# Optimization experiments

Measured on AMD Instinct MI355X. Metric: run time of the kernel, lower is better.

## Reference

```python
import jax, jax.numpy as jnp
import numpy as np
import math

HIDDEN = 1024
HEADS = 16
D_K = HIDDEN // HEADS
EPS = 1e-5


def gelu_tanh(x):
    c = math.sqrt(2.0 / math.pi)
    return 0.5 * x * (1.0 + jnp.tanh(c * (x + 0.044715 * x ** 3)))


def layer_norm(x, gamma, beta):
    mu = jnp.mean(x, axis=-1, keepdims=True)
    var = jnp.mean((x - mu) ** 2, axis=-1, keepdims=True)
    return (x - mu) * jax.lax.rsqrt(var + EPS) * gamma + beta


def setup_inputs() -> dict:
    key = jax.random.key(0)
    ks = jax.random.split(key, 12)
    s = 1.0 / math.sqrt(HIDDEN)
    s4 = 1.0 / math.sqrt(4 * HIDDEN)
    inp = {
        "x": jax.random.normal(ks[0], (2, 2048, HIDDEN), dtype=jnp.float32),
        # attention linears, stored as (in, out) so y = x @ W + b
        "Wq": jax.random.uniform(ks[1], (HIDDEN, HIDDEN), minval=-s, maxval=s),
        "bq": jax.random.uniform(ks[2], (HIDDEN,), minval=-s, maxval=s),
        "Wv": jax.random.uniform(ks[3], (HIDDEN, HIDDEN), minval=-s, maxval=s),
        "bv": jax.random.uniform(ks[4], (HIDDEN,), minval=-s, maxval=s),
        "Wo": jax.random.uniform(ks[5], (HIDDEN, HIDDEN), minval=-s, maxval=s),
        "bo": jax.random.uniform(ks[6], (HIDDEN,), minval=-s, maxval=s),
        # feed-forward
        "W1": jax.random.uniform(ks[7], (HIDDEN, 4 * HIDDEN), minval=-s, maxval=s),
        "b1": jax.random.uniform(ks[8], (4 * HIDDEN,), minval=-s, maxval=s),
        "W2": jax.random.uniform(ks[9], (4 * HIDDEN, HIDDEN), minval=-s4, maxval=s4),
        "b2": jax.random.uniform(ks[10], (HIDDEN,), minval=-s4, maxval=s4),
        # layer norms
        "g1": jnp.ones((HIDDEN,), jnp.float32),
        "beta1": jnp.zeros((HIDDEN,), jnp.float32),
        "g2": jnp.ones((HIDDEN,), jnp.float32),
        "beta2": jnp.zeros((HIDDEN,), jnp.float32),
    }
    return inp


def attention(x, Wq, bq, Wv, bv, Wo, bo):
    bs, seq, _ = x.shape
    qk = (x @ Wq + bq).reshape(bs, seq, HEADS, D_K).transpose(0, 2, 1, 3)  # b h s d
    v = (x @ Wv + bv).reshape(bs, seq, HEADS, D_K).transpose(0, 2, 1, 3)
    scores = jnp.einsum('bhqd,bhkd->bhqk', qk, qk) / math.sqrt(D_K)
    causal = jnp.tril(jnp.ones((seq, seq), dtype=bool))
    scores = jnp.where(causal[None, None], scores, -jnp.inf)
    attn = jax.nn.softmax(scores, axis=-1)
    out = jnp.einsum('bhqk,bhkd->bhqd', attn, v)
    out = out.transpose(0, 2, 1, 3).reshape(bs, seq, HIDDEN)
    return out @ Wo + bo


def reference(x, Wq, bq, Wv, bv, Wo, bo, W1, b1, W2, b2, g1, beta1, g2, beta2):
    x = x + attention(layer_norm(x, g1, beta1), Wq, bq, Wv, bv, Wo, bo)
    h = layer_norm(x, g2, beta2)
    ff = gelu_tanh(h @ W1 + b1) @ W2 + b2  # chunking is a memory detail; same math
    return x + ff
```

## Files before the change

kernel.cpp:

```cpp
#include <hip/hip_runtime.h>

typedef unsigned short u16;
typedef short bf16x8 __attribute__((ext_vector_type(8)));
typedef float f32x4 __attribute__((ext_vector_type(4)));

__device__ __forceinline__ float bf2f(u16 u) {
    union { unsigned int i; float f; } v; v.i = ((unsigned int)u) << 16; return v.f;
}
__device__ __forceinline__ u16 f2bf(float f) {
    union { float f; unsigned int i; } v; v.f = f;
    unsigned int r = v.i + 0x7fffu + ((v.i >> 16) & 1u);
    return (u16)(r >> 16);
}

__device__ __forceinline__ void gload16(const u16* g, u16* l) {
    __builtin_amdgcn_global_load_lds((__attribute__((address_space(1))) void*)(u16*)g,
                                     (__attribute__((address_space(3))) void*)l, 16, 0, 0);
}

__global__ __launch_bounds__(256) void transpose_f32_bf16(const float* __restrict__ in,
                                                          u16* __restrict__ out,
                                                          int R, int C) {
    __shared__ u16 tile[64][65];
    int c0 = blockIdx.x * 64, r0 = blockIdx.y * 64;
    for (int i = threadIdx.x; i < 4096; i += 256) {
        int r = i >> 6, c = i & 63;
        tile[r][c] = f2bf(in[(size_t)(r0 + r) * C + c0 + c]);
    }
    __syncthreads();
    for (int i = threadIdx.x; i < 4096; i += 256) {
        int r = i >> 6, c = i & 63;
        out[(size_t)(c0 + r) * R + r0 + c] = tile[c][r];
    }
}

__global__ __launch_bounds__(256) void transpose_bf16_s(const u16* __restrict__ in,
                                                        u16* __restrict__ out,
                                                        int R, int C, int istride) {
    __shared__ u16 tile[64][65];
    int c0 = blockIdx.x * 64, r0 = blockIdx.y * 64;
    in  += (size_t)blockIdx.z * R * istride;
    out += (size_t)blockIdx.z * R * C;
    for (int i = threadIdx.x; i < 4096; i += 256) {
        int r = i >> 6, c = i & 63;
        tile[r][c] = in[(size_t)(r0 + r) * istride + c0 + c];
    }
    __syncthreads();
    for (int i = threadIdx.x; i < 4096; i += 256) {
        int r = i >> 6, c = i & 63;
        out[(size_t)(c0 + r) * R + r0 + c] = tile[c][r];
    }
}

__global__ __launch_bounds__(256) void concat_bias(const float* __restrict__ a,
                                                   const float* __restrict__ b,
                                                   float* __restrict__ o) {
    int i = blockIdx.x * 256 + threadIdx.x;
    o[i] = (i < 1024) ? a[i] : b[i - 1024];
}

__global__ __launch_bounds__(256) void ln_f32(const float* __restrict__ x,
                                              const float* __restrict__ g,
                                              const float* __restrict__ be,
                                              u16* __restrict__ out) {
    int row = blockIdx.x, tid = threadIdx.x;
    int lane = tid & 63, wave = tid >> 6;
    const float* xr = x + (size_t)row * 1024 + tid * 4;
    float4 f4 = *(const float4*)xr;
    float v[4] = {f4.x, f4.y, f4.z, f4.w};
    float s1 = v[0] + v[1] + v[2] + v[3];
    float s2 = v[0]*v[0] + v[1]*v[1] + v[2]*v[2] + v[3]*v[3];
#pragma unroll
    for (int mm = 1; mm < 64; mm <<= 1) { s1 += __shfl_xor(s1, mm); s2 += __shfl_xor(s2, mm); }
    __shared__ float a1[4], a2[4];
    if (lane == 0) { a1[wave] = s1; a2[wave] = s2; }
    __syncthreads();
    s1 = a1[0] + a1[1] + a1[2] + a1[3];
    s2 = a2[0] + a2[1] + a2[2] + a2[3];
    float mean = s1 * (1.0f / 1024.0f);
    float var  = s2 * (1.0f / 1024.0f) - mean * mean;
    float rstd = rsqrtf(var + 1e-5f);
#pragma unroll
    for (int i = 0; i < 4; ++i) {
        int c = tid * 4 + i;
        float o = (v[i] - mean) * rstd * g[c] + be[c];
        out[(size_t)row * 1024 + c] = f2bf(o);
    }
}

template <int BN, int ACT, int RES, typename OutT>
__global__ __launch_bounds__(256) void gemm_gl(const u16* __restrict__ A,
                                               const u16* __restrict__ WT,
                                               const float* __restrict__ bias,
                                               const float* __restrict__ resid,
                                               OutT* __restrict__ C,
                                               int M, int N, int K, int cpx) {
    constexpr int JN = BN / 32;
    __shared__ u16 lds_a[128 * 64];
    __shared__ u16 lds_b[BN * 64];
    int tid = threadIdx.x;
    int lane = tid & 63, wave = tid >> 6;
    int l16 = lane & 15, quad = lane >> 4;
    int wm = (wave >> 1) * 64, wn = (wave & 1) * (BN / 2);

    int id = blockIdx.x;
    int slot = id >> 3;
    int bx = (id & 7) * cpx + (slot >> 5);
    int by = slot & 31;
    int m0 = by * 128, n0 = bx * BN;
    f32x4 acc[4][JN] = {};

    int scol = ((lane & 7) ^ (lane >> 3)) * 8;
    const u16* Ab = A  + (size_t)(m0 + wave * 8 + (lane >> 3)) * K + scol;
    const u16* Bb = WT + (size_t)(n0 + wave * 8 + (lane >> 3)) * K + scol;
    u16* la = lds_a + wave * 512;
    u16* lb = lds_b + wave * 512;

    int xk = (l16 & 7);

    for (int k0 = 0; k0 < K; k0 += 64) {
        __syncthreads();
#pragma unroll
        for (int it = 0; it < 4; ++it)
            gload16(Ab + (size_t)it * 32 * K + k0, la + it * 2048);
#pragma unroll
        for (int it = 0; it < JN; ++it)
            gload16(Bb + (size_t)it * 32 * K + k0, lb + it * 2048);
        __syncthreads();
#pragma unroll
        for (int s = 0; s < 2; ++s) {
            bf16x8 af[4], bfr[JN];
#pragma unroll
            for (int i = 0; i < 4; ++i)
                af[i] = *(const bf16x8*)&lds_a[(wm + i * 16 + l16) * 64 + (((s * 4 + quad) ^ xk) * 8)];
#pragma unroll
            for (int j = 0; j < JN; ++j)
                bfr[j] = *(const bf16x8*)&lds_b[(wn + j * 16 + l16) * 64 + (((s * 4 + quad) ^ xk) * 8)];
#pragma unroll
            for (int i = 0; i < 4; ++i)
#pragma unroll
                for (int j = 0; j < JN; ++j)
                    acc[i][j] = __builtin_amdgcn_mfma_f32_16x16x32_bf16(af[i], bfr[j], acc[i][j], 0, 0, 0);
        }
    }

#pragma unroll
    for (int j = 0; j < JN; ++j) {
        int col = n0 + wn + j * 16 + l16;
        float bv = bias[col];
#pragma unroll
        for (int i = 0; i < 4; ++i) {
            int rbase = m0 + wm + i * 16 + quad * 4;
#pragma unroll
            for (int r = 0; r < 4; ++r) {
                size_t idx = (size_t)(rbase + r) * N + col;
                float v = acc[i][j][r] + bv;
                if (ACT == 1) {
                    float u = v;
                    float y = 0.7978845608028654f * (u + 0.044715f * u * u * u);
                    float t = __expf(2.0f * y);
                    float th = 1.0f - 2.0f / (t + 1.0f);
                    v = 0.5f * u * (1.0f + th);
                }
                if (RES) v += resid[idx];
                if constexpr (sizeof(OutT) == 4) C[idx] = v;
                else                             C[idx] = f2bf(v);
            }
        }
    }
}

__global__ __launch_bounds__(256) void attn_kernel(const u16* __restrict__ QV,
                                                   const u16* __restrict__ Vt,
                                                   u16* __restrict__ Out) {
    int id = blockIdx.x;
    int slot = id >> 3;
    int hb = (id & 7) + 8 * (slot & 3);
    int p  = slot >> 2;
    int h = hb & 15, b = hb >> 4;
    int tid = threadIdx.x;
    int lane = tid & 63, wave = tid >> 6;
    int l16 = lane & 15, quad = lane >> 4;

    __shared__ u16 k_lds[64 * 64];
    __shared__ u16 v_lds[64 * 64];
    __shared__ u16 p_lds[4][16 * 72];

    bf16x8 ones;
#pragma unroll
    for (int e = 0; e < 8; ++e) ones[e] = (short)0x3F80;

    int srow = wave * 8 + (lane >> 3);
    int sc8  = ((lane & 7) ^ (lane >> 3)) * 8;
    int xk   = (l16 & 7);

    for (int half = 0; half < 2; ++half) {
        int t = half ? (31 - p) : p;
        int q0 = t * 64;

        const u16* qp = QV + ((size_t)b * 2048 + q0 + wave * 16 + l16) * 2048 + h * 64;
        bf16x8 qf[2];
        qf[0] = *(const bf16x8*)&qp[quad * 8];
        qf[1] = *(const bf16x8*)&qp[32 + quad * 8];

        f32x4 O[4] = {};
        f32x4 L = {};

        for (int kt = 0; kt <= t; ++kt) {
            const u16* kg = QV + ((size_t)b * 2048 + kt * 64 + srow) * 2048 + h * 64 + sc8;
            const u16* vg = Vt + ((((size_t)b * 16 + h) * 64) + srow) * 2048 + kt * 64 + sc8;
            __syncthreads();
            gload16(kg,                      k_lds + wave * 512);
            gload16(kg + (size_t)32 * 2048,  k_lds + wave * 512 + 2048);
            gload16(vg,                      v_lds + wave * 512);
            gload16(vg + (size_t)32 * 2048,  v_lds + wave * 512 + 2048);
            __syncthreads();

            f32x4 S[4] = {};
#pragma unroll
            for (int s = 0; s < 2; ++s)
#pragma unroll
                for (int j = 0; j < 4; ++j) {
                    bf16x8 kf = *(const bf16x8*)&k_lds[(j * 16 + l16) * 64 + (((s * 4 + quad) ^ xk) * 8)];
                    S[j] = __builtin_amdgcn_mfma_f32_16x16x32_bf16(qf[s], kf, S[j], 0, 0, 0);
                }

            if (kt == t) {
#pragma unroll
                for (int j = 0; j < 4; ++j) {
                    int key = j * 16 + l16;
#pragma unroll
                    for (int r = 0; r < 4; ++r)
                        if (key > wave * 16 + quad * 4 + r) S[j][r] = -1e30f;
                }
            }

#pragma unroll
            for (int j = 0; j < 4; ++j)
#pragma unroll
                for (int r = 0; r < 4; ++r) {
                    float pp = __expf(S[j][r] * 0.125f);
                    p_lds[wave][(quad * 4 + r) * 72 + j * 16 + l16] = f2bf(pp);
                }

#pragma unroll
            for (int s = 0; s < 2; ++s) {
                bf16x8 pf = *(const bf16x8*)&p_lds[wave][l16 * 72 + s * 32 + quad * 8];
                L = __builtin_amdgcn_mfma_f32_16x16x32_bf16(pf, ones, L, 0, 0, 0);
#pragma unroll
                for (int dj = 0; dj < 4; ++dj) {
                    bf16x8 vf = *(const bf16x8*)&v_lds[(dj * 16 + l16) * 64 + (((s * 4 + quad) ^ xk) * 8)];
                    O[dj] = __builtin_amdgcn_mfma_f32_16x16x32_bf16(pf, vf, O[dj], 0, 0, 0);
                }
            }
        }

#pragma unroll
        for (int r = 0; r < 4; ++r) {
            int qg = q0 + wave * 16 + quad * 4 + r;
            float inv = 1.0f / L[r];
#pragma unroll
            for (int dj = 0; dj < 4; ++dj)
                Out[((size_t)b * 2048 + qg) * 1024 + h * 64 + dj * 16 + l16] =
                    f2bf(O[dj][r] * inv);
        }
    }
}

extern "C" void kernel_launch(void* const* d_in, const int* in_sizes, int n_in,
                              void* d_out, int out_size, void* d_ws, size_t ws_size,
                              hipStream_t stream) {
    const float* x   = (const float*)d_in[0];
    const float* Wq  = (const float*)d_in[1];
    const float* bq  = (const float*)d_in[2];
    const float* Wv  = (const float*)d_in[3];
    const float* bv  = (const float*)d_in[4];
    const float* Wo  = (const float*)d_in[5];
    const float* bo  = (const float*)d_in[6];
    const float* W1  = (const float*)d_in[7];
    const float* b1  = (const float*)d_in[8];
    const float* W2  = (const float*)d_in[9];
    const float* b2  = (const float*)d_in[10];
    const float* g1  = (const float*)d_in[11];
    const float* be1 = (const float*)d_in[12];
    const float* g2  = (const float*)d_in[13];
    const float* be2 = (const float*)d_in[14];

    char* ws = (char*)d_ws;
    const size_t MB = 1 << 20;
    u16*   WqT  = (u16*)(ws + 0  * MB);
    u16*   WvT  = (u16*)(ws + 2  * MB);
    u16*   WoT  = (u16*)(ws + 4  * MB);
    u16*   W1T  = (u16*)(ws + 6  * MB);
    u16*   W2T  = (u16*)(ws + 14 * MB);
    u16*   h1   = (u16*)(ws + 22 * MB);
    u16*   QV   = (u16*)(ws + 30 * MB);
    float* x2   = (float*)(ws + 30 * MB);
    u16*   Vt   = (u16*)(ws + 46 * MB);
    u16*   ff1  = (u16*)(ws + 46 * MB);
    float* bqv  = (float*)(ws + 78 * MB);

    transpose_f32_bf16<<<dim3(16, 16), 256, 0, stream>>>(Wq, WqT, 1024, 1024);
    transpose_f32_bf16<<<dim3(16, 16), 256, 0, stream>>>(Wv, WvT, 1024, 1024);
    transpose_f32_bf16<<<dim3(16, 16), 256, 0, stream>>>(Wo, WoT, 1024, 1024);
    transpose_f32_bf16<<<dim3(64, 16), 256, 0, stream>>>(W1, W1T, 1024, 4096);
    transpose_f32_bf16<<<dim3(16, 64), 256, 0, stream>>>(W2, W2T, 4096, 1024);
    concat_bias<<<8, 256, 0, stream>>>(bq, bv, bqv);

    ln_f32<<<4096, 256, 0, stream>>>(x, g1, be1, h1);

    gemm_gl<64, 0, 0, u16><<<1024, 256, 0, stream>>>(h1, WqT, bqv, nullptr, QV, 4096, 2048, 1024, 4);

    transpose_bf16_s<<<dim3(16, 32, 2), 256, 0, stream>>>(QV + 1024, Vt, 2048, 1024, 2048);

    attn_kernel<<<512, 256, 0, stream>>>(QV, Vt, h1);

    gemm_gl<64, 0, 1, float><<<512, 256, 0, stream>>>(h1, WoT, bo, x, x2, 4096, 1024, 1024, 2);

    ln_f32<<<4096, 256, 0, stream>>>(x2, g2, be2, h1);

    gemm_gl<128, 1, 0, u16><<<1024, 256, 0, stream>>>(h1, W1T, b1, nullptr, ff1, 4096, 4096, 1024, 4);

    gemm_gl<64, 0, 1, float><<<512, 256, 0, stream>>>(ff1, W2T, b2, x2, (float*)d_out, 4096, 1024, 4096, 2);
}
```

Measured before the change: 358.6 us.

## Merge weight-prep kernels into one launch and add 256x128-tile FFN1 GEMM

Replaces the five weight-transpose launches and the bias concat with a single prep kernel that picks its job by block index. It also adds a new GEMM kernel with 256x128 output tiles and an 8x4 MFMA accumulator per wave, used for the W1+GELU matmul. The larger tile raises operand reuse per LDS load and halves the block count. In exchange it uses more registers and 48KB of LDS per block, which limits occupancy to two blocks per CU.

```diff
diff --git a/kernel.cpp b/kernel.cpp
--- a/kernel.cpp
+++ b/kernel.cpp
@@ -18,11 +18,30 @@
                                      (__attribute__((address_space(3))) void*)l, 16, 0, 0);
 }
 
-__global__ __launch_bounds__(256) void transpose_f32_bf16(const float* __restrict__ in,
-                                                          u16* __restrict__ out,
-                                                          int R, int C) {
+__global__ __launch_bounds__(256) void prep(const float* __restrict__ Wq,
+                                            const float* __restrict__ Wv,
+                                            const float* __restrict__ Wo,
+                                            const float* __restrict__ W1,
+                                            const float* __restrict__ W2,
+                                            const float* __restrict__ bq,
+                                            const float* __restrict__ bv,
+                                            u16* __restrict__ WqT, u16* __restrict__ WvT,
+                                            u16* __restrict__ WoT, u16* __restrict__ W1T,
+                                            u16* __restrict__ W2T, float* __restrict__ bqv) {
+    int id = blockIdx.x;
+    if (id >= 2816) {
+        int i = (id - 2816) * 256 + threadIdx.x;
+        bqv[i] = (i < 1024) ? bq[i] : bv[i - 1024];
+        return;
+    }
+    const float* in; u16* out; int R, C, bx, by;
+    if (id < 256)       { in = Wq; out = WqT; R = 1024; C = 1024; bx = id & 15;          by = id >> 4; }
+    else if (id < 512)  { int t = id - 256;  in = Wv; out = WvT; R = 1024; C = 1024; bx = t & 15; by = t >> 4; }
+    else if (id < 768)  { int t = id - 512;  in = Wo; out = WoT; R = 1024; C = 1024; bx = t & 15; by = t >> 4; }
+    else if (id < 1792) { int t = id - 768;  in = W1; out = W1T; R = 1024; C = 4096; bx = t & 63; by = t >> 6; }
+    else                { int t = id - 1792; in = W2; out = W2T; R = 4096; C = 1024; bx = t & 15; by = t >> 4; }
     __shared__ u16 tile[64][65];
-    int c0 = blockIdx.x * 64, r0 = blockIdx.y * 64;
+    int c0 = bx * 64, r0 = by * 64;
     for (int i = threadIdx.x; i < 4096; i += 256) {
         int r = i >> 6, c = i & 63;
         tile[r][c] = f2bf(in[(size_t)(r0 + r) * C + c0 + c]);
@@ -50,13 +69,6 @@
         int r = i >> 6, c = i & 63;
         out[(size_t)(c0 + r) * R + r0 + c] = tile[c][r];
     }
-}
-
-__global__ __launch_bounds__(256) void concat_bias(const float* __restrict__ a,
-                                                   const float* __restrict__ b,
-                                                   float* __restrict__ o) {
-    int i = blockIdx.x * 256 + threadIdx.x;
-    o[i] = (i < 1024) ? a[i] : b[i - 1024];
 }
 
 __global__ __launch_bounds__(256) void ln_f32(const float* __restrict__ x,
@@ -165,6 +177,79 @@
                 if (RES) v += resid[idx];
                 if constexpr (sizeof(OutT) == 4) C[idx] = v;
                 else                             C[idx] = f2bf(v);
+            }
+        }
+    }
+}
+
+template <int ACT>
+__global__ __launch_bounds__(256, 2) void gemm_big(const u16* __restrict__ A,
+                                                   const u16* __restrict__ WT,
+                                                   const float* __restrict__ bias,
+                                                   u16* __restrict__ C,
+                                                   int M, int N, int K) {
+    __shared__ u16 lds_a[256 * 64];
+    __shared__ u16 lds_b[128 * 64];
+    int tid = threadIdx.x;
+    int lane = tid & 63, wave = tid >> 6;
+    int l16 = lane & 15, quad = lane >> 4;
+    int wm = (wave >> 1) * 128, wn = (wave & 1) * 64;
+    int id = blockIdx.x;
+    int bx = id & 31, by = id >> 5;
+    int m0 = by * 256, n0 = bx * 128;
+    f32x4 acc[8][4] = {};
+
+    int scol = ((lane & 7) ^ (lane >> 3)) * 8;
+    const u16* Ab = A  + (size_t)(m0 + wave * 8 + (lane >> 3)) * K + scol;
+    const u16* Bb = WT + (size_t)(n0 + wave * 8 + (lane >> 3)) * K + scol;
+    u16* la = lds_a + wave * 512;
+    u16* lb = lds_b + wave * 512;
+    int xk = (l16 & 7);
+
+    for (int k0 = 0; k0 < K; k0 += 64) {
+        __syncthreads();
+#pragma unroll
+        for (int it = 0; it < 8; ++it)
+            gload16(Ab + (size_t)it * 32 * K + k0, la + it * 2048);
+#pragma unroll
+        for (int it = 0; it < 4; ++it)
+            gload16(Bb + (size_t)it * 32 * K + k0, lb + it * 2048);
+        __syncthreads();
+#pragma unroll
+        for (int s = 0; s < 2; ++s) {
+            bf16x8 bfr[4];
+#pragma unroll
+            for (int j = 0; j < 4; ++j)
+                bfr[j] = *(const bf16x8*)&lds_b[(wn + j * 16 + l16) * 64 + (((s * 4 + quad) ^ xk) * 8)];
+#pragma unroll
+            for (int i = 0; i < 8; ++i) {
+                bf16x8 af = *(const bf16x8*)&lds_a[(wm + i * 16 + l16) * 64 + (((s * 4 + quad) ^ xk) * 8)];
+#pragma unroll
+                for (int j = 0; j < 4; ++j)
+                    acc[i][j] = __builtin_amdgcn_mfma_f32_16x16x32_bf16(af, bfr[j], acc[i][j], 0, 0, 0);
+            }
+        }
+    }
+
+#pragma unroll
+    for (int j = 0; j < 4; ++j) {
+        int col = n0 + wn + j * 16 + l16;
+        float bv = bias[col];
+#pragma unroll
+        for (int i = 0; i < 8; ++i) {
+            int rbase = m0 + wm + i * 16 + quad * 4;
+#pragma unroll
+            for (int r = 0; r < 4; ++r) {
+                size_t idx = (size_t)(rbase + r) * N + col;
+                float v = acc[i][j][r] + bv;
+                if (ACT == 1) {
+                    float u = v;
+                    float y = 0.7978845608028654f * (u + 0.044715f * u * u * u);
+                    float t = __expf(2.0f * y);
+                    float th = 1.0f - 2.0f / (t + 1.0f);
+                    v = 0.5f * u * (1.0f + th);
+                }
+                C[idx] = f2bf(v);
             }
         }
     }
@@ -300,12 +385,8 @@
     u16*   ff1  = (u16*)(ws + 46 * MB);
     float* bqv  = (float*)(ws + 78 * MB);
 
-    transpose_f32_bf16<<<dim3(16, 16), 256, 0, stream>>>(Wq, WqT, 1024, 1024);
-    transpose_f32_bf16<<<dim3(16, 16), 256, 0, stream>>>(Wv, WvT, 1024, 1024);
-    transpose_f32_bf16<<<dim3(16, 16), 256, 0, stream>>>(Wo, WoT, 1024, 1024);
-    transpose_f32_bf16<<<dim3(64, 16), 256, 0, stream>>>(W1, W1T, 1024, 4096);
-    transpose_f32_bf16<<<dim3(16, 64), 256, 0, stream>>>(W2, W2T, 4096, 1024);
-    concat_bias<<<8, 256, 0, stream>>>(bq, bv, bqv);
+    prep<<<2824, 256, 0, stream>>>(Wq, Wv, Wo, W1, W2, bq, bv,
+                                   WqT, WvT, WoT, W1T, W2T, bqv);
 
     ln_f32<<<4096, 256, 0, stream>>>(x, g1, be1, h1);
 
@@ -319,7 +400,7 @@
 
     ln_f32<<<4096, 256, 0, stream>>>(x2, g2, be2, h1);
 
-    gemm_gl<128, 1, 0, u16><<<1024, 256, 0, stream>>>(h1, W1T, b1, nullptr, ff1, 4096, 4096, 1024, 4);
+    gemm_big<1><<<512, 256, 0, stream>>>(h1, W1T, b1, ff1, 4096, 4096, 1024);
 
     gemm_gl<64, 0, 1, float><<<512, 256, 0, stream>>>(ff1, W2T, b2, x2, (float*)d_out, 4096, 1024, 4096, 2);
 }
```

After: 341.3 us. 1.05x faster.
